# Kernel optimization log

Measured on AMD Instinct MI355X. Metric: run time of the kernel, lower is better.

The kernel has to match this reference:

```python
import jax, jax.numpy as jnp
import numpy as np

B, C, P, HP, WP = 128, 3, 196, 16, 16  # batch, channels, patches, patch h, patch w
E = 768  # embedding size; patches_pixel_count = C*HP*WP = 768


def setup_inputs() -> dict:
    key = jax.random.key(0)
    ks = jax.random.split(key, 9)
    return {
        "inputs": jax.random.normal(ks[0], (B, C, P, HP, WP), dtype=jnp.float32),
        "W1": jax.random.normal(ks[1], (C * HP * WP, 32), dtype=jnp.float32) * 0.02,
        "b1": jax.random.normal(ks[2], (32,), dtype=jnp.float32) * 0.02,
        "W2": jax.random.normal(ks[3], (32, 64), dtype=jnp.float32) * 0.02,
        "b2": jax.random.normal(ks[4], (64,), dtype=jnp.float32) * 0.02,
        "W3": jax.random.normal(ks[5], (64, E), dtype=jnp.float32) * 0.02,
        "b3": jax.random.normal(ks[6], (E,), dtype=jnp.float32) * 0.02,
        "cls_token": jax.random.normal(ks[7], (1, E), dtype=jnp.float32) * 0.02,
        "pos_enc": jax.random.normal(ks[8], (P + 1, E), dtype=jnp.float32) * 0.02,
    }


def reference(inputs, W1, b1, W2, b2, W3, b3, cls_token, pos_enc):
    b, c, p, hp, wp = inputs.shape
    # per-patch slab is [C, hp, wp] flattened in (C, h, w) order -> [B, P, C*hp*wp]
    x = jnp.transpose(inputs, (0, 2, 1, 3, 4)).reshape(b, p, c * hp * wp)
    x = x @ W1 + b1          # [B, P, 32]
    x = x @ W2 + b2          # [B, P, 64]
    x = x @ W3 + b3          # [B, P, E]
    cls = jnp.broadcast_to(cls_token[None], (b, 1, cls_token.shape[-1]))
    x = jnp.concatenate([cls, x], axis=1)  # [B, P+1, E]
    return x + pos_enc[None]               # broadcast add of position encodings
```

## Files before the change

kernel.cpp:

```cpp
#include <hip/hip_runtime.h>


#define BATCH 128
#define CH    3
#define NP    196
#define PIX   256
#define K1    768
#define NH    64
#define EMB   768
#define NROW  (BATCH * NP)

typedef __bf16 bf16x8 __attribute__((ext_vector_type(8)));
typedef __bf16 bf16x4 __attribute__((ext_vector_type(4)));
typedef float  f32x4  __attribute__((ext_vector_type(4)));

#define W12T_OFF 0
#define W3T_OFF  98304
#define BF_OFF   196608
#define H_OFF    199680

#define GLOAD_LDS16(g, l)                                                  \
    __builtin_amdgcn_global_load_lds(                                      \
        (const __attribute__((address_space(1))) unsigned int*)(g),        \
        (__attribute__((address_space(3))) unsigned int*)(l), 16, 0, 0)

__global__ __launch_bounds__(256) void patchembed_prep(
    const float* __restrict__ W1, const float* __restrict__ W2,
    const float* __restrict__ b1, const float* __restrict__ b2,
    const float* __restrict__ W3, const float* __restrict__ b3,
    const float* __restrict__ cls, const float* __restrict__ pos,
    __bf16* __restrict__ w12t, __bf16* __restrict__ w3t,
    float* __restrict__ bf, float* __restrict__ out)
{
    __shared__ float b12s[64];

    const int i = blockIdx.x * 256 + threadIdx.x;
    const int T0 = NH * K1;
    const int T1 = T0 + EMB;
    const int T2 = T1 + EMB * NH;

    if (i < T0) {
        const int n = i / K1, k = i - n * K1;
        float s = 0.f;
        #pragma unroll
        for (int j = 0; j < 32; ++j) s += W1[k * 32 + j] * W2[j * NH + n];
        w12t[i] = (__bf16)s;
    } else if (i < T1) {
        const int t = threadIdx.x;
        if (t < NH) {
            float s = b2[t];
            #pragma unroll
            for (int j = 0; j < 32; ++j) s += b1[j] * W2[j * NH + t];
            b12s[t] = s;
        }
        __syncthreads();
        const int c = i - T0;
        float s = b3[c];
        #pragma unroll
        for (int n = 0; n < NH; ++n) s += b12s[n] * W3[n * EMB + c];
        bf[c] = s;
    } else if (i < T2) {
        const int j = i - T1;
        const int col = j >> 6, kk = j & 63;
        w3t[j] = (__bf16)W3[kk * EMB + col];
    } else {
        const int j = i - T2;
        const int b = j / EMB, c = j - b * EMB;
        out[b * (197 * EMB) + c] = cls[c] + pos[c];
    }
}

__global__ __launch_bounds__(256, 3) void patchembed_s1(
    const float* __restrict__ X,
    const __bf16* __restrict__ w12t,
    __bf16* __restrict__ H)
{
    __shared__ __align__(16) float xs[16][772];

    const int tid  = threadIdx.x;
    const int wv   = tid >> 6;
    const int lane = tid & 63;
    const int l15  = lane & 15;
    const int q    = lane >> 4;
    const int r0   = blockIdx.x * 16;

    const int b0 = r0 / NP;
    const int p0 = r0 - b0 * NP;

    #pragma unroll
    for (int i = 0; i < 12; ++i) {
        const int chunk = wv * 12 + i;
        const int c   = chunk >> 4;
        const int row = chunk & 15;
        int p = p0 + row, b = b0;
        if (p >= NP) { p -= NP; b += 1; }
        const float* gp = X + (((b * CH) + c) * NP + p) * PIX + lane * 4;
        GLOAD_LDS16(gp, &xs[row][c * 256]);
    }
    __syncthreads();

    const __bf16* wrow = w12t + (wv * 16 + l15) * K1;
    const float*  xrow = &xs[l15][0];
    f32x4 acc = {0.f, 0.f, 0.f, 0.f};
    #pragma unroll
    for (int ks = 0; ks < 24; ++ks) {
        bf16x8 a = *(const bf16x8*)(wrow + ks * 32 + q * 8);
        const float* xp = xrow + ks * 32 + q * 8;
        f32x4 u = *(const f32x4*)xp;
        f32x4 v = *(const f32x4*)(xp + 4);
        bf16x8 xb;
        xb[0] = (__bf16)u[0]; xb[1] = (__bf16)u[1];
        xb[2] = (__bf16)u[2]; xb[3] = (__bf16)u[3];
        xb[4] = (__bf16)v[0]; xb[5] = (__bf16)v[1];
        xb[6] = (__bf16)v[2]; xb[7] = (__bf16)v[3];
        acc = __builtin_amdgcn_mfma_f32_16x16x32_bf16(a, xb, acc, 0, 0, 0);
    }
    bf16x4 hv;
    #pragma unroll
    for (int j = 0; j < 4; ++j) hv[j] = (__bf16)acc[j];
    *(bf16x4*)(H + (r0 + l15) * NH + wv * 16 + q * 4) = hv;
}

__global__ __launch_bounds__(256) void patchembed_s2(
    const __bf16* __restrict__ H,
    const __bf16* __restrict__ w3t,
    const float*  __restrict__ bf,
    const float*  __restrict__ pos,
    float* __restrict__ out)
{
    const int tid  = threadIdx.x;
    const int wv   = tid >> 6;
    const int lane = tid & 63;
    const int l15  = lane & 15;
    const int q    = lane >> 4;

    const int wave_id = blockIdx.x * 4 + wv;
    const int rt = wave_id >> 3;
    const int cs = wave_id & 7;
    const int r0 = rt * 16;

    const __bf16* hr = H + (r0 + l15) * NH;
    bf16x8 hb0 = *(const bf16x8*)(hr + q * 8);
    bf16x8 hb1 = *(const bf16x8*)(hr + 32 + q * 8);

    const int row = r0 + l15;
    const int b = row / NP, p = row - b * NP;
    float* orow = out + (b * 197 + p + 1) * EMB;
    const float* prow = pos + (p + 1) * EMB;

    #pragma unroll
    for (int t = 0; t < 6; ++t) {
        const int colb = cs * 96 + t * 16;
        const __bf16* wr = w3t + (colb + l15) * NH;
        bf16x8 wa0 = *(const bf16x8*)(wr + q * 8);
        bf16x8 wa1 = *(const bf16x8*)(wr + 32 + q * 8);
        f32x4 z = {0.f, 0.f, 0.f, 0.f};
        f32x4 c = __builtin_amdgcn_mfma_f32_16x16x32_bf16(wa0, hb0, z, 0, 0, 0);
        c       = __builtin_amdgcn_mfma_f32_16x16x32_bf16(wa1, hb1, c, 0, 0, 0);
        const int c4 = colb + q * 4;
        f32x4 pv = *(const f32x4*)(prow + c4);
        f32x4 bv = *(const f32x4*)(bf + c4);
        *(f32x4*)(orow + c4) = c + pv + bv;
    }
}

extern "C" void kernel_launch(void* const* d_in, const int* in_sizes, int n_in,
                              void* d_out, int out_size, void* d_ws, size_t ws_size,
                              hipStream_t stream)
{
    const float* X   = (const float*)d_in[0];
    const float* W1  = (const float*)d_in[1];
    const float* b1  = (const float*)d_in[2];
    const float* W2  = (const float*)d_in[3];
    const float* b2  = (const float*)d_in[4];
    const float* W3  = (const float*)d_in[5];
    const float* b3  = (const float*)d_in[6];
    const float* cls = (const float*)d_in[7];
    const float* pos = (const float*)d_in[8];
    float* out = (float*)d_out;

    char* ws = (char*)d_ws;
    __bf16* w12t = (__bf16*)(ws + W12T_OFF);
    __bf16* w3t  = (__bf16*)(ws + W3T_OFF);
    float*  bf   = (float*)(ws + BF_OFF);
    __bf16* H    = (__bf16*)(ws + H_OFF);

    patchembed_prep<<<771, 256, 0, stream>>>(W1, W2, b1, b2, W3, b3, cls, pos,
                                             w12t, w3t, bf, out);
    patchembed_s1<<<NROW / 16, 256, 0, stream>>>(X, w12t, H);
    patchembed_s2<<<NROW / 16 * 2, 256, 0, stream>>>(H, w3t, bf, pos, out);
}
```

Measured before the change: 194.0 us.

## Fuse both GEMM stages into one kernel via shared-memory hidden tile

Merges the first-stage kernel (patch × fused W1W2) and the second-stage kernel (hidden × W3 plus bias and position add) into one launch. The 16×64 bf16 hidden tile now stays in shared memory instead of going to a global workspace, and each wave computes 192 output columns. This removes one kernel launch and the global write and read of H. In exchange, the second stage runs with fewer waves, the same number of blocks as stage one, each doing more work, which may reduce latency hiding on the output-store-bound phase.

Measured after the change: 192.4 us. About the same (-0.8%).

```diff
diff --git a/kernel.cpp b/kernel.cpp
--- a/kernel.cpp
+++ b/kernel.cpp
@@ -17,7 +17,6 @@
 #define W12T_OFF 0
 #define W3T_OFF  98304
 #define BF_OFF   196608
-#define H_OFF    199680
 
 #define GLOAD_LDS16(g, l)                                                  \
     __builtin_amdgcn_global_load_lds(                                      \
@@ -70,12 +69,16 @@
     }
 }
 
-__global__ __launch_bounds__(256, 3) void patchembed_s1(
+__global__ __launch_bounds__(256, 3) void patchembed_main(
     const float* __restrict__ X,
     const __bf16* __restrict__ w12t,
-    __bf16* __restrict__ H)
+    const __bf16* __restrict__ w3t,
+    const float*  __restrict__ bf,
+    const float*  __restrict__ pos,
+    float* __restrict__ out)
 {
-    __shared__ __align__(16) float xs[16][772];
+    __shared__ __align__(16) float  xs[16][772];
+    __shared__ __align__(16) __bf16 h2s[16][72];
 
     const int tid  = threadIdx.x;
     const int wv   = tid >> 6;
@@ -99,68 +102,53 @@
     }
     __syncthreads();
 
-    const __bf16* wrow = w12t + (wv * 16 + l15) * K1;
-    const float*  xrow = &xs[l15][0];
-    f32x4 acc = {0.f, 0.f, 0.f, 0.f};
-    #pragma unroll
-    for (int ks = 0; ks < 24; ++ks) {
-        bf16x8 a = *(const bf16x8*)(wrow + ks * 32 + q * 8);
-        const float* xp = xrow + ks * 32 + q * 8;
-        f32x4 u = *(const f32x4*)xp;
-        f32x4 v = *(const f32x4*)(xp + 4);
-        bf16x8 xb;
-        xb[0] = (__bf16)u[0]; xb[1] = (__bf16)u[1];
-        xb[2] = (__bf16)u[2]; xb[3] = (__bf16)u[3];
-        xb[4] = (__bf16)v[0]; xb[5] = (__bf16)v[1];
-        xb[6] = (__bf16)v[2]; xb[7] = (__bf16)v[3];
-        acc = __builtin_amdgcn_mfma_f32_16x16x32_bf16(a, xb, acc, 0, 0, 0);
+    {
+        const __bf16* wrow = w12t + (wv * 16 + l15) * K1;
+        const float*  xrow = &xs[l15][0];
+        f32x4 acc = {0.f, 0.f, 0.f, 0.f};
+        #pragma unroll
+        for (int ks = 0; ks < 24; ++ks) {
+            bf16x8 a = *(const bf16x8*)(wrow + ks * 32 + q * 8);
+            const float* xp = xrow + ks * 32 + q * 8;
+            f32x4 u = *(const f32x4*)xp;
+            f32x4 v = *(const f32x4*)(xp + 4);
+            bf16x8 xb;
+            xb[0] = (__bf16)u[0]; xb[1] = (__bf16)u[1];
+            xb[2] = (__bf16)u[2]; xb[3] = (__bf16)u[3];
+            xb[4] = (__bf16)v[0]; xb[5] = (__bf16)v[1];
+            xb[6] = (__bf16)v[2]; xb[7] = (__bf16)v[3];
+            acc = __builtin_amdgcn_mfma_f32_16x16x32_bf16(a, xb, acc, 0, 0, 0);
+        }
+        bf16x4 hv;
+        #pragma unroll
+        for (int j = 0; j < 4; ++j) hv[j] = (__bf16)acc[j];
+        *(bf16x4*)(&h2s[l15][wv * 16 + q * 4]) = hv;
     }
-    bf16x4 hv;
-    #pragma unroll
-    for (int j = 0; j < 4; ++j) hv[j] = (__bf16)acc[j];
-    *(bf16x4*)(H + (r0 + l15) * NH + wv * 16 + q * 4) = hv;
-}
+    __syncthreads();
 
-__global__ __launch_bounds__(256) void patchembed_s2(
-    const __bf16* __restrict__ H,
-    const __bf16* __restrict__ w3t,
-    const float*  __restrict__ bf,
-    const float*  __restrict__ pos,
-    float* __restrict__ out)
-{
-    const int tid  = threadIdx.x;
-    const int wv   = tid >> 6;
-    const int lane = tid & 63;
-    const int l15  = lane & 15;
-    const int q    = lane >> 4;
+    {
+        bf16x8 hb0 = *(const bf16x8*)(&h2s[l15][q * 8]);
+        bf16x8 hb1 = *(const bf16x8*)(&h2s[l15][32 + q * 8]);
 
-    const int wave_id = blockIdx.x * 4 + wv;
-    const int rt = wave_id >> 3;
-    const int cs = wave_id & 7;
-    const int r0 = rt * 16;
+        const int row = r0 + l15;
+        const int b = row / NP, p = row - b * NP;
+        float* orow = out + (b * 197 + p + 1) * EMB;
+        const float* prow = pos + (p + 1) * EMB;
 
-    const __bf16* hr = H + (r0 + l15) * NH;
-    bf16x8 hb0 = *(const bf16x8*)(hr + q * 8);
-    bf16x8 hb1 = *(const bf16x8*)(hr + 32 + q * 8);
-
-    const int row = r0 + l15;
-    const int b = row / NP, p = row - b * NP;
-    float* orow = out + (b * 197 + p + 1) * EMB;
-    const float* prow = pos + (p + 1) * EMB;
-
-    #pragma unroll
-    for (int t = 0; t < 6; ++t) {
-        const int colb = cs * 96 + t * 16;
-        const __bf16* wr = w3t + (colb + l15) * NH;
-        bf16x8 wa0 = *(const bf16x8*)(wr + q * 8);
-        bf16x8 wa1 = *(const bf16x8*)(wr + 32 + q * 8);
-        f32x4 z = {0.f, 0.f, 0.f, 0.f};
-        f32x4 c = __builtin_amdgcn_mfma_f32_16x16x32_bf16(wa0, hb0, z, 0, 0, 0);
-        c       = __builtin_amdgcn_mfma_f32_16x16x32_bf16(wa1, hb1, c, 0, 0, 0);
-        const int c4 = colb + q * 4;
-        f32x4 pv = *(const f32x4*)(prow + c4);
-        f32x4 bv = *(const f32x4*)(bf + c4);
-        *(f32x4*)(orow + c4) = c + pv + bv;
+        #pragma unroll 4
+        for (int t = 0; t < 12; ++t) {
+            const int colb = wv * 192 + t * 16;
+            const __bf16* wr = w3t + (colb + l15) * NH;
+            bf16x8 wa0 = *(const bf16x8*)(wr + q * 8);
+            bf16x8 wa1 = *(const bf16x8*)(wr + 32 + q * 8);
+            f32x4 z = {0.f, 0.f, 0.f, 0.f};
+            f32x4 c = __builtin_amdgcn_mfma_f32_16x16x32_bf16(wa0, hb0, z, 0, 0, 0);
+            c       = __builtin_amdgcn_mfma_f32_16x16x32_bf16(wa1, hb1, c, 0, 0, 0);
+            const int c4 = colb + q * 4;
+            f32x4 pv = *(const f32x4*)(prow + c4);
+            f32x4 bv = *(const f32x4*)(bf + c4);
+            *(f32x4*)(orow + c4) = c + pv + bv;
+        }
     }
 }
 
@@ -183,10 +171,8 @@
     __bf16* w12t = (__bf16*)(ws + W12T_OFF);
     __bf16* w3t  = (__bf16*)(ws + W3T_OFF);
     float*  bf   = (float*)(ws + BF_OFF);
-    __bf16* H    = (__bf16*)(ws + H_OFF);
 
     patchembed_prep<<<771, 256, 0, stream>>>(W1, W2, b1, b2, W3, b3, cls, pos,
                                              w12t, w3t, bf, out);
-    patchembed_s1<<<NROW / 16, 256, 0, stream>>>(X, w12t, H);
-    patchembed_s2<<<NROW / 16 * 2, 256, 0, stream>>>(H, w3t, bf, pos, out);
+    patchembed_main<<<NROW / 16, 256, 0, stream>>>(X, w12t, w3t, bf, pos, out);
 }
```
